# Optimization experiments

Measured on AMD Instinct MI355X. Metric: run time of the kernel, lower is better.

## Reference

```python
import jax, jax.numpy as jnp
import numpy as np

B, C, H, W = 4, 128, 64, 64
CO = 128

def setup_inputs() -> dict:
    key = jax.random.key(0)
    ks = jax.random.split(key, 10)
    s = 1.0 / np.sqrt(C)
    return {
        "x":  jax.random.normal(ks[0], (B, C, H, W), dtype=jnp.float32),
        "Wq": jax.random.uniform(ks[1], (C, C), jnp.float32, -s, s),
        "bq": jax.random.uniform(ks[2], (C,), jnp.float32, -s, s),
        "Wk": jax.random.uniform(ks[3], (C, C), jnp.float32, -s, s),
        "bk": jax.random.uniform(ks[4], (C,), jnp.float32, -s, s),
        "Wv": jax.random.uniform(ks[5], (C, C), jnp.float32, -s, s),
        "bv": jax.random.uniform(ks[6], (C,), jnp.float32, -s, s),
        "gamma": jnp.ones((1,), dtype=jnp.float32),
        "Wo": jax.random.uniform(ks[7], (CO, C), jnp.float32, -s, s),
        "bo": jax.random.uniform(ks[8], (CO,), jnp.float32, -s, s),
    }

def reference(x, Wq, bq, Wk, bk, Wv, bv, gamma, Wo, bo):
    b, c, h, w = x.shape
    xf = x.reshape(b, c, h * w)                       # [B,C,N]
    # 1x1 convs == channel matmuls
    Q = jnp.einsum('oc,bcn->bon', Wq, xf) + bq[None, :, None]
    K = jnp.einsum('oc,bcn->bon', Wk, xf) + bk[None, :, None]
    V = jnp.einsum('oc,bcn->bon', Wv, xf) + bv[None, :, None]
    # attention[b,i,j] = softmax_j( sum_c Q[b,c,i] K[b,c,j] )  (unscaled)
    scores = jnp.einsum('bci,bcj->bij', Q, K)         # [B,N,N]
    attn = jax.nn.softmax(scores, axis=-1)
    # selfAtten[b,c,i] = sum_j V[b,c,j] attn[b,i,j]
    sa = jnp.einsum('bcj,bij->bci', V, attn)          # [B,C,N]
    sa = gamma[0] * sa + xf
    out = jnp.einsum('oc,bcn->bon', Wo, sa) + bo[None, :, None]
    return out.reshape(b, Wo.shape[0], h, w)
```

## Files before the change

kernel.cpp:

```cpp
#include <hip/hip_runtime.h>

#define BB 4
#define CC 128
#define NN 4096

typedef float f32x4 __attribute__((ext_vector_type(4)));
typedef __bf16 bf16x8 __attribute__((ext_vector_type(8)));

#define MFMA16(A, B, C) __builtin_amdgcn_mfma_f32_16x16x32_bf16((A), (B), (C), 0, 0, 0)

typedef __attribute__((address_space(3))) void lds_void;
typedef __attribute__((address_space(1))) void glob_void;
#define GLD16(g, l) __builtin_amdgcn_global_load_lds((const glob_void*)(g), (lds_void*)(l), 16, 0, 0)

__device__ __forceinline__ int fK(int r) { return (r & 3) | (((r >> 3) & 1) << 2); }

__global__ __launch_bounds__(256)
void pack_w(const float* __restrict__ Wq, const float* __restrict__ bq,
            const float* __restrict__ Wk, const float* __restrict__ bk,
            const float* __restrict__ Wv, const float* __restrict__ bv,
            const float* __restrict__ Wo, const float* __restrict__ bo,
            __bf16* __restrict__ Wpk, float* __restrict__ bpk)
{
    const int mat = blockIdx.x >> 3;
    const int p   = blockIdx.x & 7;
    const int tid = threadIdx.x;
    const int ks  = tid >> 6;
    const int lane = tid & 63;
    const int col = lane & 15;
    const int quad = lane >> 4;

    const float LOG2E = 1.44269504088896340736f;
    const float* W = (mat == 0) ? Wq : (mat == 1) ? Wk : (mat == 2) ? Wv : Wo;
    const float* bsrc = (mat == 0) ? bq : (mat == 1) ? bk : (mat == 2) ? bv : bo;
    const float scale = (mat == 0) ? LOG2E : 1.0f;

    const float* wr = W + (size_t)(p * 16 + col) * CC + ks * 32 + quad * 8;
    float4 f0 = *(const float4*)wr;
    float4 f1 = *(const float4*)(wr + 4);
    bf16x8 a;
    a[0]=(__bf16)(f0.x*scale); a[1]=(__bf16)(f0.y*scale);
    a[2]=(__bf16)(f0.z*scale); a[3]=(__bf16)(f0.w*scale);
    a[4]=(__bf16)(f1.x*scale); a[5]=(__bf16)(f1.y*scale);
    a[6]=(__bf16)(f1.z*scale); a[7]=(__bf16)(f1.w*scale);
    *(bf16x8*)&Wpk[(((size_t)(mat * 8 + p) * 4 + ks) * 64 + lane) * 8] = a;

    if (p == 0 && tid < 128) bpk[mat * 128 + tid] = bsrc[tid] * scale;
}

__global__ __launch_bounds__(512, 2)
void qkv_gemm(const float* __restrict__ x,
              const __bf16* __restrict__ Wpk, const float* __restrict__ bpk,
              __bf16* __restrict__ Qt, __bf16* __restrict__ Kt,
              __bf16* __restrict__ Vblk)
{
    const int b    = blockIdx.y;
    const int n0   = blockIdx.x * 32;
    const int tid  = threadIdx.x;
    const int lane = tid & 63;
    const int wv   = __builtin_amdgcn_readfirstlane(tid >> 6);
    const int col  = lane & 15;
    const int quad = lane >> 4;

    __shared__ __bf16 xs[32 * 144];
    __shared__ __bf16 vs[128 * 32];

    {
        const int n  = tid & 31;
        const int c0 = tid >> 5;
        const float* xb = x + ((size_t)b * CC) * NN + n0 + n;
#pragma unroll
        for (int i = 0; i < 4; i++) {
            int c = (c0 + i * 16) * 2;
            float v0 = xb[(size_t)c * NN];
            float v1 = xb[(size_t)(c + 1) * NN];
            union { __bf16 h[2]; unsigned u; } pk;
            pk.h[0] = (__bf16)v0; pk.h[1] = (__bf16)v1;
            *(unsigned*)&xs[n * 144 + c] = pk.u;
        }
    }
    __syncthreads();

    bf16x8 Bf[2][4];
#pragma unroll
    for (int ng = 0; ng < 2; ng++)
#pragma unroll
        for (int ks = 0; ks < 4; ks++)
            Bf[ng][ks] = *(const bf16x8*)&xs[(ng * 16 + col) * 144 + ks * 32 + quad * 8];

#pragma unroll 1
    for (int mat = 0; mat < 3; mat++) {
        const int pg = wv;
        const int o0 = pg * 16;

        bf16x8 Af[4];
#pragma unroll
        for (int ks = 0; ks < 4; ks++)
            Af[ks] = *(const bf16x8*)&Wpk[(((size_t)(mat * 8 + pg) * 4 + ks) * 64 + lane) * 8];

        f32x4 D[2];
#pragma unroll
        for (int ng = 0; ng < 2; ng++) D[ng] = (f32x4){0.f, 0.f, 0.f, 0.f};
#pragma unroll
        for (int ks = 0; ks < 4; ks++)
#pragma unroll
            for (int ng = 0; ng < 2; ng++)
                D[ng] = MFMA16(Af[ks], Bf[ng][ks], D[ng]);

        float4 bias = *(const float4*)(bpk + mat * 128 + o0 + quad * 4);

#pragma unroll
        for (int ng = 0; ng < 2; ng++) {
            const int n = ng * 16 + col;
            float v[4];
#pragma unroll
            for (int r = 0; r < 4; r++)
                v[r] = D[ng][r] + ((const float*)&bias)[r];
            if (mat == 0) {
                union { __bf16 h[4]; uint2 u; } pk;
                for (int r = 0; r < 4; r++) pk.h[r] = (__bf16)v[r];
                *(uint2*)&Qt[((size_t)b * NN + n0 + n) * CC + o0 + quad * 4] = pk.u;
            } else if (mat == 1) {
                const int rin = ((n0 & 32) + n) & 63;
                const int chunk = ((o0 + quad * 4) >> 3) ^ fK(rin);
                union { __bf16 h[4]; uint2 u; } pk;
                for (int r = 0; r < 4; r++) pk.h[r] = (__bf16)v[r];
                *(uint2*)&Kt[((size_t)b * NN + n0 + n) * CC + chunk * 8 + (quad & 1) * 4] = pk.u;
            } else {
#pragma unroll
                for (int r = 0; r < 4; r++)
                    vs[(o0 + quad * 4 + r) * 32 + n] = (__bf16)v[r];
            }
        }
    }
    __syncthreads();

    {
        __bf16* vd = Vblk + (((size_t)b * 64 + (n0 >> 6)) * CC) * 64;
        const int chbase = (n0 & 32) >> 3;
        int idx = tid;
        int c = idx >> 2, chl = idx & 3;
        bf16x8 v = *(const bf16x8*)&vs[c * 32 + chl * 8];
        *(bf16x8*)&vd[c * 64 + (((chbase + chl) ^ (c & 7)) * 8)] = v;
    }
}

__global__ __launch_bounds__(256, 2)
void flash_attn(const __bf16* __restrict__ Qt, const __bf16* __restrict__ Kt,
                const __bf16* __restrict__ Vblk,
                __bf16* __restrict__ Opart, float* __restrict__ Lpart)
{
    const int blk = blockIdx.x;
    const int b   = blk & 3;
    const int jhi = (blk >> 2) & 1;
    const int rr  = blk >> 3;
    const int js  = jhi * 2 + (rr & 1);
    const int it  = rr >> 1;
    const int i0  = it * 128;

    const int tid  = threadIdx.x;
    const int lane = tid & 63;
    const int iw   = __builtin_amdgcn_readfirstlane(tid >> 6);
    const int col  = lane & 15;
    const int quad = lane >> 4;

    __shared__ __align__(16) char smem[65536];

    const __bf16* Qb = Qt + (size_t)b * NN * CC;
    const char*   Ks = (const char*)(Kt + (size_t)b * NN * CC);
    const char*   Vs = (const char*)(Vblk + ((size_t)b * 64 * CC) * 64);

    const int ibase = i0 + iw * 32;

    bf16x8 qf[2][4];
#pragma unroll
    for (int ig = 0; ig < 2; ig++)
#pragma unroll
        for (int ks = 0; ks < 4; ks++)
            qf[ig][ks] = *(const bf16x8*)(Qb + (size_t)(ibase + ig * 16 + col) * CC
                                             + ks * 32 + quad * 8);

    const int perm = ((col & 12) << 1) | (col & 3);
    const int fR   = fK(perm);
    int kaddr[4][4];
    const int joff[4] = {0, 4, 32, 36};
#pragma unroll
    for (int jg = 0; jg < 4; jg++)
#pragma unroll
        for (int ks = 0; ks < 4; ks++)
            kaddr[jg][ks] = (perm + joff[jg]) * 256 + (((ks * 4 + quad) ^ fR) * 16);
    int vaddr[8][2];
#pragma unroll
    for (int cg = 0; cg < 8; cg++)
#pragma unroll
        for (int t = 0; t < 2; t++)
            vaddr[cg][t] = 16384 + (cg * 16 + col) * 128 + (((t * 4 + quad) ^ (col & 7)) * 16);

    f32x4 O[2][8];
    float lrun[2] = {0.f, 0.f};
#pragma unroll
    for (int ig = 0; ig < 2; ig++)
#pragma unroll
        for (int cg = 0; cg < 8; cg++) O[ig][cg] = (f32x4){0.f, 0.f, 0.f, 0.f};

    {
        const char* kg = Ks + (size_t)(js * 16) * 16384;
        const char* vg = Vs + (size_t)(js * 16) * 16384;
#pragma unroll
        for (int q = 0; q < 4; q++) {
            const int call = iw * 4 + q;
            GLD16(kg + call * 1024 + lane * 16, smem + call * 1024 + lane * 16);
            GLD16(vg + call * 1024 + lane * 16, smem + 16384 + call * 1024 + lane * 16);
        }
    }

#pragma unroll 1
    for (int t16 = 0; t16 < 16; t16++) {
        __syncthreads();

        char* Buf = smem + (t16 & 1) * 32768;

        if (t16 < 15) {
            const int jt = js * 16 + t16 + 1;
            const char* kg = Ks + (size_t)jt * 16384;
            const char* vg = Vs + (size_t)jt * 16384;
            char* kd = smem + ((t16 + 1) & 1) * 32768;
#pragma unroll
            for (int q = 0; q < 4; q++) {
                const int call = iw * 4 + q;
                GLD16(kg + call * 1024 + lane * 16, kd + call * 1024 + lane * 16);
                GLD16(vg + call * 1024 + lane * 16, kd + 16384 + call * 1024 + lane * 16);
            }
        }

        f32x4 S[2][4];
#pragma unroll
        for (int ig = 0; ig < 2; ig++)
#pragma unroll
            for (int jg = 0; jg < 4; jg++)
                S[ig][jg] = (f32x4){-32.f, -32.f, -32.f, -32.f};
#pragma unroll
        for (int ks = 0; ks < 4; ks++) {
            bf16x8 k0 = *(const bf16x8*)(Buf + kaddr[0][ks]);
            bf16x8 k1 = *(const bf16x8*)(Buf + kaddr[1][ks]);
            bf16x8 k2 = *(const bf16x8*)(Buf + kaddr[2][ks]);
            bf16x8 k3 = *(const bf16x8*)(Buf + kaddr[3][ks]);
            S[0][0] = MFMA16(k0, qf[0][ks], S[0][0]);
            S[1][0] = MFMA16(k0, qf[1][ks], S[1][0]);
            S[0][1] = MFMA16(k1, qf[0][ks], S[0][1]);
            S[1][1] = MFMA16(k1, qf[1][ks], S[1][1]);
            S[0][2] = MFMA16(k2, qf[0][ks], S[0][2]);
            S[1][2] = MFMA16(k2, qf[1][ks], S[1][2]);
            S[0][3] = MFMA16(k3, qf[0][ks], S[0][3]);
            S[1][3] = MFMA16(k3, qf[1][ks], S[1][3]);
        }

        float s0 = 0.f, s1 = 0.f;
#pragma unroll
        for (int jg = 0; jg < 4; jg++)
#pragma unroll
            for (int r = 0; r < 4; r++) {
                float p0 = __builtin_amdgcn_exp2f(S[0][jg][r]);
                float p1 = __builtin_amdgcn_exp2f(S[1][jg][r]);
                S[0][jg][r] = p0; s0 += p0;
                S[1][jg][r] = p1; s1 += p1;
            }
        lrun[0] += s0;
        lrun[1] += s1;

#pragma unroll
        for (int t = 0; t < 2; t++) {
            bf16x8 pf0, pf1;
#pragma unroll
            for (int e = 0; e < 8; e++) {
                int jg = 2 * t + (e >> 2), r = e & 3;
                pf0[e] = (__bf16)S[0][jg][r];
                pf1[e] = (__bf16)S[1][jg][r];
            }
#pragma unroll
            for (int cg = 0; cg < 8; cg++) {
                bf16x8 vf = *(const bf16x8*)(Buf + vaddr[cg][t]);
                O[0][cg] = MFMA16(vf, pf0, O[0][cg]);
                O[1][cg] = MFMA16(vf, pf1, O[1][cg]);
            }
        }
    }
    __syncthreads();

    __bf16* Ol = (__bf16*)smem;
#pragma unroll
    for (int ig = 0; ig < 2; ig++) {
        lrun[ig] += __shfl_xor(lrun[ig], 16);
        lrun[ig] += __shfl_xor(lrun[ig], 32);
#pragma unroll
        for (int cg = 0; cg < 8; cg++)
#pragma unroll
            for (int r = 0; r < 4; r++)
                Ol[(cg * 16 + quad * 4 + r) * 136 + iw * 32 + ig * 16 + col]
                    = (__bf16)O[ig][cg][r];
        if (quad == 0)
            Lpart[((size_t)b * 4 + js) * NN + i0 + iw * 32 + ig * 16 + col] = lrun[ig];
    }
    __syncthreads();
    {
        __bf16* Od = Opart + ((size_t)((b * 4 + js) * 32 + it) * CC) * 128;
#pragma unroll
        for (int e = 0; e < 8; e++) {
            int u = e * 256 + tid;
            int c = u >> 4, ch = u & 15;
            *(uint4*)&Od[c * 128 + ch * 8] = *(const uint4*)&Ol[c * 136 + ch * 8];
        }
    }
}

__global__ __launch_bounds__(256, 2)
void proj_out(const __bf16* __restrict__ Opart, const float* __restrict__ Lpart,
              const float* __restrict__ x,
              const __bf16* __restrict__ Wpk, const float* __restrict__ bpk,
              const float* __restrict__ gamma, float* __restrict__ out)
{
    const int b    = blockIdx.y;
    const int n0   = blockIdx.x * 32;
    const int tid  = threadIdx.x;
    const int lane = tid & 63;
    const int wv   = __builtin_amdgcn_readfirstlane(tid >> 6);
    const int col  = lane & 15;
    const int quad = lane >> 4;

    __shared__ __bf16 sas[32 * 144];
    __shared__ float  outs[128 * 34];

    const float g = gamma[0];

    {
        const int n  = tid & 31;
        const int c0 = tid >> 5;
        const int it = n0 >> 7;
        const int io = (n0 & 127) + n;
        float l = 0.f;
#pragma unroll
        for (int jsp = 0; jsp < 4; jsp++)
            l += Lpart[((size_t)b * 4 + jsp) * NN + n0 + n];
        const float gl = g / l;
        const float* xb = x + ((size_t)b * CC) * NN + n0 + n;
        const __bf16* Ob = Opart + ((size_t)(b * 4) * 32 + it) * CC * 128;
#pragma unroll
        for (int i = 0; i < 8; i++) {
            int c = (c0 + i * 8) * 2;
            float s0 = 0.f, s1 = 0.f;
#pragma unroll
            for (int jsp = 0; jsp < 4; jsp++) {
                const __bf16* p = Ob + (size_t)jsp * (32 * CC * 128) + c * 128 + io;
                s0 += (float)p[0];
                s1 += (float)p[128];
            }
            float v0 = xb[(size_t)c * NN] + s0 * gl;
            float v1 = xb[(size_t)(c + 1) * NN] + s1 * gl;
            union { __bf16 h[2]; unsigned u; } pk;
            pk.h[0] = (__bf16)v0; pk.h[1] = (__bf16)v1;
            *(unsigned*)&sas[n * 144 + c] = pk.u;
        }
    }
    __syncthreads();

    bf16x8 Bf[2][4];
#pragma unroll
    for (int ng = 0; ng < 2; ng++)
#pragma unroll
        for (int ks = 0; ks < 4; ks++)
            Bf[ng][ks] = *(const bf16x8*)&sas[(ng * 16 + col) * 144 + ks * 32 + quad * 8];

#pragma unroll
    for (int p = 0; p < 2; p++) {
        const int pg = wv * 2 + p;
        const int o0 = pg * 16;
        bf16x8 Af[4];
#pragma unroll
        for (int ks = 0; ks < 4; ks++)
            Af[ks] = *(const bf16x8*)&Wpk[(((size_t)(3 * 8 + pg) * 4 + ks) * 64 + lane) * 8];

        f32x4 D[2];
#pragma unroll
        for (int ng = 0; ng < 2; ng++) D[ng] = (f32x4){0.f, 0.f, 0.f, 0.f};
#pragma unroll
        for (int ks = 0; ks < 4; ks++)
#pragma unroll
            for (int ng = 0; ng < 2; ng++)
                D[ng] = MFMA16(Af[ks], Bf[ng][ks], D[ng]);

        float4 bias = *(const float4*)(bpk + 3 * 128 + o0 + quad * 4);
#pragma unroll
        for (int ng = 0; ng < 2; ng++)
#pragma unroll
            for (int r = 0; r < 4; r++)
                outs[(o0 + quad * 4 + r) * 34 + ng * 16 + col]
                    = D[ng][r] + ((const float*)&bias)[r];
    }
    __syncthreads();

    {
        float* od = out + ((size_t)b * CC) * NN + n0;
#pragma unroll
        for (int e = 0; e < 16; e++) {
            int k = e * 256 + tid;
            int o = k >> 5, n = k & 31;
            od[(size_t)o * NN + n] = outs[o * 34 + n];
        }
    }
}

extern "C" void kernel_launch(void* const* d_in, const int* in_sizes, int n_in,
                              void* d_out, int out_size, void* d_ws, size_t ws_size,
                              hipStream_t stream)
{
    const float* x  = (const float*)d_in[0];
    const float* Wq = (const float*)d_in[1];
    const float* bq = (const float*)d_in[2];
    const float* Wk = (const float*)d_in[3];
    const float* bk = (const float*)d_in[4];
    const float* Wv = (const float*)d_in[5];
    const float* bv = (const float*)d_in[6];
    const float* gm = (const float*)d_in[7];
    const float* Wo = (const float*)d_in[8];
    const float* bo = (const float*)d_in[9];

    __bf16* Qt    = (__bf16*)d_ws;
    __bf16* Kt    = Qt + (size_t)BB * NN * CC;
    __bf16* Vblk  = Kt + (size_t)BB * NN * CC;
    __bf16* Opart = Vblk + (size_t)BB * NN * CC;
    float*  Lpart = (float*)(Opart + (size_t)16 * 32 * CC * 128);
    __bf16* Wpk   = (__bf16*)(Lpart + (size_t)16 * NN);
    float*  bpk   = (float*)(Wpk + 4 * 8 * 4 * 64 * 8);
    float*  out   = (float*)d_out;

    pack_w<<<32, 256, 0, stream>>>(Wq, bq, Wk, bk, Wv, bv, Wo, bo, Wpk, bpk);
    qkv_gemm<<<dim3(128, 4), 512, 0, stream>>>(x, Wpk, bpk, Qt, Kt, Vblk);
    flash_attn<<<512, 256, 0, stream>>>(Qt, Kt, Vblk, Opart, Lpart);
    proj_out<<<dim3(128, 4), 256, 0, stream>>>(Opart, Lpart, x, Wpk, bpk, gm, out);
}
```

Baseline: 127.6 us.

## Load K fragments directly from global into registers, shrink LDS to V only

K tiles no longer go through double-buffered LDS. Each wave now loads its K fragments straight from global memory into registers, one tile ahead, and the swizzled K layout in the projection kernel becomes a plain row-major layout. LDS drops to the V double buffer, about 34 KB, which could allow more resident blocks per CU. The cost is four waves per block reading the same K rows from global/L2 instead of sharing them in LDS, plus extra registers for the prefetched fragments.

```diff
diff --git a/kernel.cpp b/kernel.cpp
--- a/kernel.cpp
+++ b/kernel.cpp
@@ -12,8 +12,6 @@
 typedef __attribute__((address_space(3))) void lds_void;
 typedef __attribute__((address_space(1))) void glob_void;
 #define GLD16(g, l) __builtin_amdgcn_global_load_lds((const glob_void*)(g), (lds_void*)(l), 16, 0, 0)
-
-__device__ __forceinline__ int fK(int r) { return (r & 3) | (((r >> 3) & 1) << 2); }
 
 __global__ __launch_bounds__(256)
 void pack_w(const float* __restrict__ Wq, const float* __restrict__ bq,
@@ -116,16 +114,11 @@
 #pragma unroll
             for (int r = 0; r < 4; r++)
                 v[r] = D[ng][r] + ((const float*)&bias)[r];
-            if (mat == 0) {
+            if (mat < 2) {
+                __bf16* dst = (mat == 0) ? Qt : Kt;
                 union { __bf16 h[4]; uint2 u; } pk;
                 for (int r = 0; r < 4; r++) pk.h[r] = (__bf16)v[r];
-                *(uint2*)&Qt[((size_t)b * NN + n0 + n) * CC + o0 + quad * 4] = pk.u;
-            } else if (mat == 1) {
-                const int rin = ((n0 & 32) + n) & 63;
-                const int chunk = ((o0 + quad * 4) >> 3) ^ fK(rin);
-                union { __bf16 h[4]; uint2 u; } pk;
-                for (int r = 0; r < 4; r++) pk.h[r] = (__bf16)v[r];
-                *(uint2*)&Kt[((size_t)b * NN + n0 + n) * CC + chunk * 8 + (quad & 1) * 4] = pk.u;
+                *(uint2*)&dst[((size_t)b * NN + n0 + n) * CC + o0 + quad * 4] = pk.u;
             } else {
 #pragma unroll
                 for (int r = 0; r < 4; r++)
@@ -164,10 +157,10 @@
     const int col  = lane & 15;
     const int quad = lane >> 4;
 
-    __shared__ __align__(16) char smem[65536];
+    __shared__ __align__(16) char smem[34816];
 
     const __bf16* Qb = Qt + (size_t)b * NN * CC;
-    const char*   Ks = (const char*)(Kt + (size_t)b * NN * CC);
+    const __bf16* Kb = Kt + (size_t)b * NN * CC;
     const char*   Vs = (const char*)(Vblk + ((size_t)b * 64 * CC) * 64);
 
     const int ibase = i0 + iw * 32;
@@ -181,20 +174,15 @@
                                              + ks * 32 + quad * 8);
 
     const int perm = ((col & 12) << 1) | (col & 3);
-    const int fR   = fK(perm);
-    int kaddr[4][4];
-    const int joff[4] = {0, 4, 32, 36};
-#pragma unroll
-    for (int jg = 0; jg < 4; jg++)
-#pragma unroll
-        for (int ks = 0; ks < 4; ks++)
-            kaddr[jg][ks] = (perm + joff[jg]) * 256 + (((ks * 4 + quad) ^ fR) * 16);
+    const __bf16* krA = Kb + (size_t)(js * 1024 + perm) * CC + quad * 8;
+    const __bf16* krC = krA + 32 * CC;
+
     int vaddr[8][2];
 #pragma unroll
     for (int cg = 0; cg < 8; cg++)
 #pragma unroll
         for (int t = 0; t < 2; t++)
-            vaddr[cg][t] = 16384 + (cg * 16 + col) * 128 + (((t * 4 + quad) ^ (col & 7)) * 16);
+            vaddr[cg][t] = (cg * 16 + col) * 128 + (((t * 4 + quad) ^ (col & 7)) * 16);
 
     f32x4 O[2][8];
     float lrun[2] = {0.f, 0.f};
@@ -203,14 +191,21 @@
 #pragma unroll
         for (int cg = 0; cg < 8; cg++) O[ig][cg] = (f32x4){0.f, 0.f, 0.f, 0.f};
 
-    {
-        const char* kg = Ks + (size_t)(js * 16) * 16384;
+    bf16x8 kf[4][4];
+#pragma unroll
+    for (int ks = 0; ks < 4; ks++) {
+        kf[0][ks] = *(const bf16x8*)((const char*)krA + ks * 64);
+        kf[1][ks] = *(const bf16x8*)((const char*)krA + 1024 + ks * 64);
+        kf[2][ks] = *(const bf16x8*)((const char*)krC + ks * 64);
+        kf[3][ks] = *(const bf16x8*)((const char*)krC + 1024 + ks * 64);
+    }
+
+    {
         const char* vg = Vs + (size_t)(js * 16) * 16384;
 #pragma unroll
         for (int q = 0; q < 4; q++) {
             const int call = iw * 4 + q;
-            GLD16(kg + call * 1024 + lane * 16, smem + call * 1024 + lane * 16);
-            GLD16(vg + call * 1024 + lane * 16, smem + 16384 + call * 1024 + lane * 16);
+            GLD16(vg + call * 1024 + lane * 16, smem + call * 1024 + lane * 16);
         }
     }
 
@@ -218,18 +213,15 @@
     for (int t16 = 0; t16 < 16; t16++) {
         __syncthreads();
 
-        char* Buf = smem + (t16 & 1) * 32768;
+        char* Vb = smem + (t16 & 1) * 16384;
 
         if (t16 < 15) {
-            const int jt = js * 16 + t16 + 1;
-            const char* kg = Ks + (size_t)jt * 16384;
-            const char* vg = Vs + (size_t)jt * 16384;
-            char* kd = smem + ((t16 + 1) & 1) * 32768;
+            const char* vg = Vs + (size_t)(js * 16 + t16 + 1) * 16384;
+            char* vd = smem + ((t16 + 1) & 1) * 16384;
 #pragma unroll
             for (int q = 0; q < 4; q++) {
                 const int call = iw * 4 + q;
-                GLD16(kg + call * 1024 + lane * 16, kd + call * 1024 + lane * 16);
-                GLD16(vg + call * 1024 + lane * 16, kd + 16384 + call * 1024 + lane * 16);
+                GLD16(vg + call * 1024 + lane * 16, vd + call * 1024 + lane * 16);
             }
         }
 
@@ -241,18 +233,26 @@
                 S[ig][jg] = (f32x4){-32.f, -32.f, -32.f, -32.f};
 #pragma unroll
         for (int ks = 0; ks < 4; ks++) {
-            bf16x8 k0 = *(const bf16x8*)(Buf + kaddr[0][ks]);
-            bf16x8 k1 = *(const bf16x8*)(Buf + kaddr[1][ks]);
-            bf16x8 k2 = *(const bf16x8*)(Buf + kaddr[2][ks]);
-            bf16x8 k3 = *(const bf16x8*)(Buf + kaddr[3][ks]);
-            S[0][0] = MFMA16(k0, qf[0][ks], S[0][0]);
-            S[1][0] = MFMA16(k0, qf[1][ks], S[1][0]);
-            S[0][1] = MFMA16(k1, qf[0][ks], S[0][1]);
-            S[1][1] = MFMA16(k1, qf[1][ks], S[1][1]);
-            S[0][2] = MFMA16(k2, qf[0][ks], S[0][2]);
-            S[1][2] = MFMA16(k2, qf[1][ks], S[1][2]);
-            S[0][3] = MFMA16(k3, qf[0][ks], S[0][3]);
-            S[1][3] = MFMA16(k3, qf[1][ks], S[1][3]);
+            S[0][0] = MFMA16(kf[0][ks], qf[0][ks], S[0][0]);
+            S[1][0] = MFMA16(kf[0][ks], qf[1][ks], S[1][0]);
+            S[0][1] = MFMA16(kf[1][ks], qf[0][ks], S[0][1]);
+            S[1][1] = MFMA16(kf[1][ks], qf[1][ks], S[1][1]);
+            S[0][2] = MFMA16(kf[2][ks], qf[0][ks], S[0][2]);
+            S[1][2] = MFMA16(kf[2][ks], qf[1][ks], S[1][2]);
+            S[0][3] = MFMA16(kf[3][ks], qf[0][ks], S[0][3]);
+            S[1][3] = MFMA16(kf[3][ks], qf[1][ks], S[1][3]);
+        }
+
+        krA += 64 * CC;
+        krC += 64 * CC;
+        if (t16 < 15) {
+#pragma unroll
+            for (int ks = 0; ks < 4; ks++) {
+                kf[0][ks] = *(const bf16x8*)((const char*)krA + ks * 64);
+                kf[1][ks] = *(const bf16x8*)((const char*)krA + 1024 + ks * 64);
+                kf[2][ks] = *(const bf16x8*)((const char*)krC + ks * 64);
+                kf[3][ks] = *(const bf16x8*)((const char*)krC + 1024 + ks * 64);
+            }
         }
 
         float s0 = 0.f, s1 = 0.f;
@@ -279,7 +279,7 @@
             }
 #pragma unroll
             for (int cg = 0; cg < 8; cg++) {
-                bf16x8 vf = *(const bf16x8*)(Buf + vaddr[cg][t]);
+                bf16x8 vf = *(const bf16x8*)(Vb + vaddr[cg][t]);
                 O[0][cg] = MFMA16(vf, pf0, O[0][cg]);
                 O[1][cg] = MFMA16(vf, pf1, O[1][cg]);
             }
```

New measurement: 164.7 us. +29.0%, slower.

## Split each key tile across two wave groups in flash attention

Applied to the files above, without the earlier changes.

Doubles the flash_attn block to 512 threads. Each group of four waves now handles half of every 64-key tile: 32 keys for the score MFMAs and the matching half of the P·V reduction. The two groups' partial O accumulators and row sums are combined through fp32 shared memory at the end before being written as bf16. This gives more waves per CU to hide latency and halves per-wave score work, at the cost of a larger LDS footprint, an extra reduction pass, and duplicated Q fragments in registers.

```diff
diff --git a/kernel.cpp b/kernel.cpp
--- a/kernel.cpp
+++ b/kernel.cpp
@@ -145,7 +145,7 @@
     }
 }
 
-__global__ __launch_bounds__(256, 2)
+__global__ __launch_bounds__(512, 4)
 void flash_attn(const __bf16* __restrict__ Qt, const __bf16* __restrict__ Kt,
                 const __bf16* __restrict__ Vblk,
                 __bf16* __restrict__ Opart, float* __restrict__ Lpart)
@@ -160,11 +160,13 @@
 
     const int tid  = threadIdx.x;
     const int lane = tid & 63;
-    const int iw   = __builtin_amdgcn_readfirstlane(tid >> 6);
+    const int wv   = __builtin_amdgcn_readfirstlane(tid >> 6);
+    const int iw   = wv & 3;
+    const int jw   = wv >> 2;
     const int col  = lane & 15;
     const int quad = lane >> 4;
 
-    __shared__ __align__(16) char smem[65536];
+    __shared__ __align__(16) char smem[69632];
 
     const __bf16* Qb = Qt + (size_t)b * NN * CC;
     const char*   Ks = (const char*)(Kt + (size_t)b * NN * CC);
@@ -182,19 +184,16 @@
 
     const int perm = ((col & 12) << 1) | (col & 3);
     const int fR   = fK(perm);
-    int kaddr[4][4];
-    const int joff[4] = {0, 4, 32, 36};
-#pragma unroll
-    for (int jg = 0; jg < 4; jg++)
-#pragma unroll
-        for (int ks = 0; ks < 4; ks++)
-            kaddr[jg][ks] = (perm + joff[jg]) * 256 + (((ks * 4 + quad) ^ fR) * 16);
-    int vaddr[8][2];
+    int kaddr[2][4];
+#pragma unroll
+    for (int jg = 0; jg < 2; jg++)
+#pragma unroll
+        for (int ks = 0; ks < 4; ks++)
+            kaddr[jg][ks] = (perm + jw * 32 + 4 * jg) * 256 + (((ks * 4 + quad) ^ fR) * 16);
+    int vaddr[8];
 #pragma unroll
     for (int cg = 0; cg < 8; cg++)
-#pragma unroll
-        for (int t = 0; t < 2; t++)
-            vaddr[cg][t] = 16384 + (cg * 16 + col) * 128 + (((t * 4 + quad) ^ (col & 7)) * 16);
+        vaddr[cg] = (cg * 16 + col) * 128 + (((jw * 4 + quad) ^ (col & 7)) * 16);
 
     f32x4 O[2][8];
     float lrun[2] = {0.f, 0.f};
@@ -207,8 +206,8 @@
         const char* kg = Ks + (size_t)(js * 16) * 16384;
         const char* vg = Vs + (size_t)(js * 16) * 16384;
 #pragma unroll
-        for (int q = 0; q < 4; q++) {
-            const int call = iw * 4 + q;
+        for (int q = 0; q < 2; q++) {
+            const int call = wv * 2 + q;
             GLD16(kg + call * 1024 + lane * 16, smem + call * 1024 + lane * 16);
             GLD16(vg + call * 1024 + lane * 16, smem + 16384 + call * 1024 + lane * 16);
         }
@@ -226,38 +225,32 @@
             const char* vg = Vs + (size_t)jt * 16384;
             char* kd = smem + ((t16 + 1) & 1) * 32768;
 #pragma unroll
-            for (int q = 0; q < 4; q++) {
-                const int call = iw * 4 + q;
+            for (int q = 0; q < 2; q++) {
+                const int call = wv * 2 + q;
                 GLD16(kg + call * 1024 + lane * 16, kd + call * 1024 + lane * 16);
                 GLD16(vg + call * 1024 + lane * 16, kd + 16384 + call * 1024 + lane * 16);
             }
         }
 
-        f32x4 S[2][4];
+        f32x4 S[2][2];
 #pragma unroll
         for (int ig = 0; ig < 2; ig++)
 #pragma unroll
-            for (int jg = 0; jg < 4; jg++)
+            for (int jg = 0; jg < 2; jg++)
                 S[ig][jg] = (f32x4){-32.f, -32.f, -32.f, -32.f};
 #pragma unroll
         for (int ks = 0; ks < 4; ks++) {
             bf16x8 k0 = *(const bf16x8*)(Buf + kaddr[0][ks]);
             bf16x8 k1 = *(const bf16x8*)(Buf + kaddr[1][ks]);
-            bf16x8 k2 = *(const bf16x8*)(Buf + kaddr[2][ks]);
-            bf16x8 k3 = *(const bf16x8*)(Buf + kaddr[3][ks]);
             S[0][0] = MFMA16(k0, qf[0][ks], S[0][0]);
             S[1][0] = MFMA16(k0, qf[1][ks], S[1][0]);
             S[0][1] = MFMA16(k1, qf[0][ks], S[0][1]);
             S[1][1] = MFMA16(k1, qf[1][ks], S[1][1]);
-            S[0][2] = MFMA16(k2, qf[0][ks], S[0][2]);
-            S[1][2] = MFMA16(k2, qf[1][ks], S[1][2]);
-            S[0][3] = MFMA16(k3, qf[0][ks], S[0][3]);
-            S[1][3] = MFMA16(k3, qf[1][ks], S[1][3]);
         }
 
         float s0 = 0.f, s1 = 0.f;
 #pragma unroll
-        for (int jg = 0; jg < 4; jg++)
+        for (int jg = 0; jg < 2; jg++)
 #pragma unroll
             for (int r = 0; r < 4; r++) {
                 float p0 = __builtin_amdgcn_exp2f(S[0][jg][r]);
@@ -268,48 +261,66 @@
         lrun[0] += s0;
         lrun[1] += s1;
 
-#pragma unroll
-        for (int t = 0; t < 2; t++) {
-            bf16x8 pf0, pf1;
-#pragma unroll
-            for (int e = 0; e < 8; e++) {
-                int jg = 2 * t + (e >> 2), r = e & 3;
-                pf0[e] = (__bf16)S[0][jg][r];
-                pf1[e] = (__bf16)S[1][jg][r];
-            }
-#pragma unroll
-            for (int cg = 0; cg < 8; cg++) {
-                bf16x8 vf = *(const bf16x8*)(Buf + vaddr[cg][t]);
-                O[0][cg] = MFMA16(vf, pf0, O[0][cg]);
-                O[1][cg] = MFMA16(vf, pf1, O[1][cg]);
-            }
-        }
-    }
-    __syncthreads();
-
-    __bf16* Ol = (__bf16*)smem;
+        bf16x8 pf0, pf1;
+#pragma unroll
+        for (int e = 0; e < 8; e++) {
+            int jg = e >> 2, r = e & 3;
+            pf0[e] = (__bf16)S[0][jg][r];
+            pf1[e] = (__bf16)S[1][jg][r];
+        }
+        char* Vb = Buf + 16384;
+#pragma unroll
+        for (int cg = 0; cg < 8; cg++) {
+            bf16x8 vf = *(const bf16x8*)(Vb + vaddr[cg]);
+            O[0][cg] = MFMA16(vf, pf0, O[0][cg]);
+            O[1][cg] = MFMA16(vf, pf1, O[1][cg]);
+        }
+    }
+    __syncthreads();
+
+    float* Om = (float*)smem;
+    float* lb = (float*)(smem + 67584);
+
 #pragma unroll
     for (int ig = 0; ig < 2; ig++) {
         lrun[ig] += __shfl_xor(lrun[ig], 16);
         lrun[ig] += __shfl_xor(lrun[ig], 32);
-#pragma unroll
-        for (int cg = 0; cg < 8; cg++)
-#pragma unroll
-            for (int r = 0; r < 4; r++)
-                Ol[(cg * 16 + quad * 4 + r) * 136 + iw * 32 + ig * 16 + col]
-                    = (__bf16)O[ig][cg][r];
-        if (quad == 0)
-            Lpart[((size_t)b * 4 + js) * NN + i0 + iw * 32 + ig * 16 + col] = lrun[ig];
+        if (quad == 0) lb[jw * 128 + iw * 32 + ig * 16 + col] = lrun[ig];
+    }
+    if (jw == 0) {
+#pragma unroll
+        for (int ig = 0; ig < 2; ig++)
+#pragma unroll
+            for (int cg = 0; cg < 8; cg++)
+#pragma unroll
+                for (int r = 0; r < 4; r++)
+                    Om[(cg * 16 + quad * 4 + r) * 132 + iw * 32 + ig * 16 + col] = O[ig][cg][r];
+    }
+    __syncthreads();
+    if (jw == 1) {
+#pragma unroll
+        for (int ig = 0; ig < 2; ig++)
+#pragma unroll
+            for (int cg = 0; cg < 8; cg++)
+#pragma unroll
+                for (int r = 0; r < 4; r++)
+                    Om[(cg * 16 + quad * 4 + r) * 132 + iw * 32 + ig * 16 + col] += O[ig][cg][r];
     }
     __syncthreads();
     {
         __bf16* Od = Opart + ((size_t)((b * 4 + js) * 32 + it) * CC) * 128;
 #pragma unroll
-        for (int e = 0; e < 8; e++) {
-            int u = e * 256 + tid;
+        for (int e = 0; e < 4; e++) {
+            int u = e * 512 + tid;
             int c = u >> 4, ch = u & 15;
-            *(uint4*)&Od[c * 128 + ch * 8] = *(const uint4*)&Ol[c * 136 + ch * 8];
-        }
+            const float* src = Om + c * 132 + ch * 8;
+            union { __bf16 h[8]; uint4 v; } pk;
+#pragma unroll
+            for (int k = 0; k < 8; k++) pk.h[k] = (__bf16)src[k];
+            *(uint4*)&Od[c * 128 + ch * 8] = pk.v;
+        }
+        if (tid < 128)
+            Lpart[((size_t)b * 4 + js) * NN + i0 + tid] = lb[tid] + lb[128 + tid];
     }
 }
 
@@ -435,6 +446,6 @@
 
     pack_w<<<32, 256, 0, stream>>>(Wq, bq, Wk, bk, Wv, bv, Wo, bo, Wpk, bpk);
     qkv_gemm<<<dim3(128, 4), 512, 0, stream>>>(x, Wpk, bpk, Qt, Kt, Vblk);
-    flash_attn<<<512, 256, 0, stream>>>(Qt, Kt, Vblk, Opart, Lpart);
+    flash_attn<<<512, 512, 0, stream>>>(Qt, Kt, Vblk, Opart, Lpart);
     proj_out<<<dim3(128, 4), 256, 0, stream>>>(Opart, Lpart, x, Wpk, bpk, gm, out);
 }
```

Measured after the change: 135.5 us. 1.06x slower.
